# Kernel tuning notes

Hardware: AMD Instinct MI355X
Metric: run time of the kernel (lower is better)

## Reference

```python
import jax, jax.numpy as jnp
import numpy as np

BN_EPS = 1e-5


def sparsemax(z):
    # z: [B, D]; sparse projection onto the simplex along last axis.
    D = z.shape[-1]
    z_sorted = jnp.flip(jnp.sort(z, axis=-1), axis=-1)          # descending
    cs = jnp.cumsum(z_sorted, axis=-1)                           # cumulative sums
    k = jnp.arange(1, D + 1, dtype=z.dtype)                      # 1..D
    support = (1.0 + k * z_sorted) > cs                          # support condition
    k_star = jnp.sum(support, axis=-1, keepdims=True)            # support size, int
    cs_k = jnp.take_along_axis(cs, k_star - 1, axis=-1)
    tau = (cs_k - 1.0) / k_star.astype(z.dtype)                  # threshold
    return jnp.maximum(z - tau, 0.0)


def setup_inputs() -> dict:
    key = jax.random.key(0)
    k1, k2, k3 = jax.random.split(key, 3)
    B, D = 32768, 1024
    a = jax.random.normal(k1, (B, D), dtype=jnp.float32)
    p = jax.random.uniform(k2, (B, D), dtype=jnp.float32)        # prior scales in (0,1)
    W = jax.random.normal(k3, (D, D), dtype=jnp.float32) * (1.0 / np.sqrt(D))
    b = jnp.zeros((D,), dtype=jnp.float32)
    gamma = jnp.ones((D,), dtype=jnp.float32)
    beta = jnp.zeros((D,), dtype=jnp.float32)
    return {"a": a, "p": p, "W": W, "b": b, "gamma": gamma, "beta": beta}


def reference(a, p, W, b, gamma, beta):
    # Linear: a @ W^T + b  (torch nn.Linear convention)
    h = jnp.einsum("bd,ed->be", a, W) + b
    # BatchNorm1d (training mode: batch stats, biased variance)
    mean = jnp.mean(h, axis=0)
    var = jnp.mean(jnp.square(h - mean), axis=0)
    h = (h - mean) * jax.lax.rsqrt(var + BN_EPS) * gamma + beta
    # Prior scaling, then sparsemax -> attention mask
    mask = sparsemax(p * h)
    return mask
```

## Files before the change

### kernel.cpp

```cpp
#include <hip/hip_runtime.h>
#include <hip/hip_fp16.h>
#include <stdint.h>

typedef _Float16 f16x8 __attribute__((ext_vector_type(8)));
typedef float f32x4 __attribute__((ext_vector_type(4)));

#define BM 128
#define BN 128
#define BK 64

__device__ __forceinline__ void async_copy16(const void* g, void* l) {
  __builtin_amdgcn_global_load_lds(
      (__attribute__((address_space(1))) void*)(g),
      (__attribute__((address_space(3))) void*)(l),
      16, 0, 0);
}

__global__ __launch_bounds__(256) void cvt_f32_f16(const float* __restrict__ in,
                                                   _Float16* __restrict__ out,
                                                   size_t n) {
  size_t i = ((size_t)blockIdx.x * 256 + threadIdx.x) * 8;
  if (i + 8 > n) return;
  float4 u = *(const float4*)(in + i);
  float4 v = *(const float4*)(in + i + 4);
  f16x8 h;
  h[0] = (_Float16)u.x; h[1] = (_Float16)u.y; h[2] = (_Float16)u.z; h[3] = (_Float16)u.w;
  h[4] = (_Float16)v.x; h[5] = (_Float16)v.y; h[6] = (_Float16)v.z; h[7] = (_Float16)v.w;
  *(f16x8*)(out + i) = h;
}

template <bool DIRECT>
__global__ __launch_bounds__(256) void gemm_f16(const _Float16* __restrict__ Ah,
                                                const _Float16* __restrict__ Wh,
                                                const float* __restrict__ Af,
                                                const float* __restrict__ Wf,
                                                const float* __restrict__ bias,
                                                float* __restrict__ C,
                                                float* __restrict__ sum,
                                                float* __restrict__ sumsq,
                                                int M, int N, int K) {
  __shared__ __attribute__((aligned(16))) _Float16 lsA[BM * BK];
  __shared__ __attribute__((aligned(16))) _Float16 lsB[BN * BK];

  const int tid  = threadIdx.x;
  const int wave = tid >> 6;
  const int lane = tid & 63;
  const int wrow = (wave >> 1) * 64;
  const int wcol = (wave & 1) * 64;
  const int l16  = lane & 15;
  const int quad = lane >> 4;
  const int bm = blockIdx.y * BM;
  const int bn = blockIdx.x * BN;

  f32x4 acc[4][4];
#pragma unroll
  for (int i = 0; i < 4; ++i)
#pragma unroll
    for (int j = 0; j < 4; ++j) acc[i][j] = (f32x4){0.f, 0.f, 0.f, 0.f};

  for (int k0 = 0; k0 < K; k0 += BK) {
    if constexpr (DIRECT) {
#pragma unroll
      for (int i = 0; i < 4; ++i) {
        const int basechunk = i * 256 + wave * 64;
        const int g   = basechunk + lane;
        const int row = g >> 3;
        const int kc  = ((g & 7) ^ (row & 7)) << 3;
        async_copy16(Ah + (size_t)(bm + row) * K + k0 + kc, &lsA[basechunk * 8]);
        async_copy16(Wh + (size_t)(bn + row) * K + k0 + kc, &lsB[basechunk * 8]);
      }
    } else {
#pragma unroll
      for (int i = 0; i < 4; ++i) {
        const int g   = i * 256 + tid;
        const int row = g >> 3;
        const int kc  = ((g & 7) ^ (row & 7)) << 3;
        {
          const float* src = Af + (size_t)(bm + row) * K + k0 + kc;
          float4 u = *(const float4*)src;
          float4 v = *(const float4*)(src + 4);
          f16x8 h;
          h[0] = (_Float16)u.x; h[1] = (_Float16)u.y; h[2] = (_Float16)u.z; h[3] = (_Float16)u.w;
          h[4] = (_Float16)v.x; h[5] = (_Float16)v.y; h[6] = (_Float16)v.z; h[7] = (_Float16)v.w;
          *(f16x8*)&lsA[g * 8] = h;
        }
        {
          const float* src = Wf + (size_t)(bn + row) * K + k0 + kc;
          float4 u = *(const float4*)src;
          float4 v = *(const float4*)(src + 4);
          f16x8 h;
          h[0] = (_Float16)u.x; h[1] = (_Float16)u.y; h[2] = (_Float16)u.z; h[3] = (_Float16)u.w;
          h[4] = (_Float16)v.x; h[5] = (_Float16)v.y; h[6] = (_Float16)v.z; h[7] = (_Float16)v.w;
          *(f16x8*)&lsB[g * 8] = h;
        }
      }
    }
    __syncthreads();

#pragma unroll
    for (int kk = 0; kk < BK; kk += 32) {
      f16x8 af[4], bf[4];
#pragma unroll
      for (int i = 0; i < 4; ++i) {
        const int r = wrow + i * 16 + l16;
        const int col = ((kk >> 3) + quad) ^ (l16 & 7);
        af[i] = *(const f16x8*)&lsA[r * 64 + col * 8];
      }
#pragma unroll
      for (int j = 0; j < 4; ++j) {
        const int r = wcol + j * 16 + l16;
        const int col = ((kk >> 3) + quad) ^ (l16 & 7);
        bf[j] = *(const f16x8*)&lsB[r * 64 + col * 8];
      }
#pragma unroll
      for (int i = 0; i < 4; ++i)
#pragma unroll
        for (int j = 0; j < 4; ++j)
          acc[i][j] = __builtin_amdgcn_mfma_f32_16x16x32_f16(af[i], bf[j], acc[i][j], 0, 0, 0);
    }
    __syncthreads();
  }

#pragma unroll
  for (int j = 0; j < 4; ++j) {
    const int c = bn + wcol + j * 16 + l16;
    const float bv = bias[c];
    float s = 0.f, s2 = 0.f;
#pragma unroll
    for (int i = 0; i < 4; ++i) {
      const int r = bm + wrow + i * 16 + quad * 4;
      float* Cp = C + (size_t)r * N + c;
      f32x4 v = acc[i][j];
#pragma unroll
      for (int rr = 0; rr < 4; ++rr) {
        float val = v[rr] + bv;
        Cp[(size_t)rr * N] = val;
        s += val;
        s2 += val * val;
      }
    }
    s  += __shfl_xor(s, 16, 64);  s  += __shfl_xor(s, 32, 64);
    s2 += __shfl_xor(s2, 16, 64); s2 += __shfl_xor(s2, 32, 64);
    if (quad == 0) {
      atomicAdd(&sum[c], s);
      atomicAdd(&sumsq[c], s2);
    }
  }
}

__global__ __launch_bounds__(256) void bn_finalize(const float* __restrict__ sum,
                                                   const float* __restrict__ sumsq,
                                                   const float* __restrict__ gamma,
                                                   const float* __restrict__ beta,
                                                   float* __restrict__ scale,
                                                   float* __restrict__ shift,
                                                   float invB) {
  const int c = blockIdx.x * 256 + threadIdx.x;
  float mean = sum[c] * invB;
  float var  = sumsq[c] * invB - mean * mean;
  float rstd = rsqrtf(var + 1e-5f);
  float sc = rstd * gamma[c];
  scale[c] = sc;
  shift[c] = beta[c] - mean * sc;
}

__global__ __launch_bounds__(256) void bn_sparsemax(const float* H,
                                                    const float* __restrict__ P,
                                                    const float* __restrict__ scale,
                                                    const float* __restrict__ shift,
                                                    float* out, int D) {
  const int wave = threadIdx.x >> 6;
  const int lane = threadIdx.x & 63;
  const int row = blockIdx.x * 4 + wave;
  const size_t rowoff = (size_t)row * D;

  const f32x4* H4 = (const f32x4*)(H + rowoff);
  const f32x4* P4 = (const f32x4*)(P + rowoff);
  const f32x4* SC = (const f32x4*)scale;
  const f32x4* SH = (const f32x4*)shift;

  f32x4 z[4];
  float tot = 0.f;
#pragma unroll
  for (int j = 0; j < 4; ++j) {
    const int idx = j * 64 + lane;
    f32x4 zz = P4[idx] * (H4[idx] * SC[idx] + SH[idx]);
    z[j] = zz;
    tot += zz[0] + zz[1] + zz[2] + zz[3];
  }
#pragma unroll
  for (int o = 32; o > 0; o >>= 1) tot += __shfl_xor(tot, o, 64);

  float tau = (tot - 1.0f) / (float)D;
  float kprev = -1.0f;
  for (int it = 0; it < 64; ++it) {
    float s = 0.f, kf = 0.f;
#pragma unroll
    for (int j = 0; j < 4; ++j)
#pragma unroll
      for (int c = 0; c < 4; ++c) {
        float zz = z[j][c];
        if (zz > tau) { s += zz; kf += 1.0f; }
      }
#pragma unroll
    for (int o = 32; o > 0; o >>= 1) {
      s  += __shfl_xor(s, o, 64);
      kf += __shfl_xor(kf, o, 64);
    }
    tau = (s - 1.0f) / kf;
    if (kf == kprev) break;
    kprev = kf;
  }

  f32x4* O4 = (f32x4*)(out + rowoff);
#pragma unroll
  for (int j = 0; j < 4; ++j) {
    const int idx = j * 64 + lane;
    f32x4 o;
#pragma unroll
    for (int c = 0; c < 4; ++c) o[c] = fmaxf(z[j][c] - tau, 0.f);
    O4[idx] = o;
  }
}

extern "C" void kernel_launch(void* const* d_in, const int* in_sizes, int n_in,
                              void* d_out, int out_size, void* d_ws, size_t ws_size,
                              hipStream_t stream) {
  const float* a     = (const float*)d_in[0];
  const float* p     = (const float*)d_in[1];
  const float* W     = (const float*)d_in[2];
  const float* b     = (const float*)d_in[3];
  const float* gamma = (const float*)d_in[4];
  const float* beta  = (const float*)d_in[5];
  float* out = (float*)d_out;

  const int D = in_sizes[3];
  const int Brows = in_sizes[0] / D;
  const int K = D, N = D;

  float* wsum   = (float*)d_ws;
  float* wsumsq = wsum + D;
  float* wscale = wsum + 2 * D;
  float* wshift = wsum + 3 * D;
  _Float16* Ah = (_Float16*)((char*)d_ws + 16384);
  _Float16* Wh = Ah + (size_t)Brows * D;
  const size_t need = 16384 + ((size_t)Brows * D + (size_t)D * D) * sizeof(_Float16);
  const bool direct = ws_size >= need;

  hipMemsetAsync(d_ws, 0, 2 * D * sizeof(float), stream);

  if (direct) {
    const size_t na = (size_t)Brows * D;
    const size_t nw = (size_t)D * D;
    cvt_f32_f16<<<dim3((unsigned)(na / 8 / 256)), 256, 0, stream>>>(a, Ah, na);
    cvt_f32_f16<<<dim3((unsigned)(nw / 8 / 256)), 256, 0, stream>>>(W, Wh, nw);
    gemm_f16<true><<<dim3(N / BN, Brows / BM), 256, 0, stream>>>(
        Ah, Wh, nullptr, nullptr, b, out, wsum, wsumsq, Brows, N, K);
  } else {
    gemm_f16<false><<<dim3(N / BN, Brows / BM), 256, 0, stream>>>(
        nullptr, nullptr, a, W, b, out, wsum, wsumsq, Brows, N, K);
  }

  bn_finalize<<<dim3(D / 256), 256, 0, stream>>>(wsum, wsumsq, gamma, beta, wscale, wshift,
                                                 1.0f / (float)Brows);
  bn_sparsemax<<<dim3(Brows / 4), 256, 0, stream>>>(out, p, wscale, wshift, out, D);
}
```

Baseline: 464.1 us.

## Store GEMM output as fp16, replace stat atomics with partials, remap tiles per XCD

The GEMM now writes the pre-BN activations as fp16 into a workspace buffer, so the write and the later read in the sparsemax kernel move half as many bytes. Per-column sum and sum-of-squares atomics are replaced by per-tile partial slots, which a new finalize kernel reduces. This also removes the memset. Block indices are remapped so that consecutive M-tiles land on the same XCD, to improve L2 reuse. Rounding H to fp16 adds precision loss before the batch-norm and sparsemax steps.

```diff
diff --git a/kernel.cpp b/kernel.cpp
--- a/kernel.cpp
+++ b/kernel.cpp
@@ -3,6 +3,7 @@
 #include <stdint.h>
 
 typedef _Float16 f16x8 __attribute__((ext_vector_type(8)));
+typedef _Float16 f16x4 __attribute__((ext_vector_type(4)));
 typedef float f32x4 __attribute__((ext_vector_type(4)));
 
 #define BM 128
@@ -29,19 +30,117 @@
   *(f16x8*)(out + i) = h;
 }
 
-template <bool DIRECT>
-__global__ __launch_bounds__(256) void gemm_f16(const _Float16* __restrict__ Ah,
-                                                const _Float16* __restrict__ Wh,
-                                                const float* __restrict__ Af,
-                                                const float* __restrict__ Wf,
-                                                const float* __restrict__ bias,
-                                                float* __restrict__ C,
-                                                float* __restrict__ sum,
-                                                float* __restrict__ sumsq,
-                                                int M, int N, int K) {
+template <bool H16>
+__global__ __launch_bounds__(256) void gemm_direct(const _Float16* __restrict__ Ah,
+                                                   const _Float16* __restrict__ Wh,
+                                                   const float* __restrict__ bias,
+                                                   void* __restrict__ Hout,
+                                                   float* __restrict__ psum,
+                                                   float* __restrict__ psumsq,
+                                                   int M, int N, int K) {
   __shared__ __attribute__((aligned(16))) _Float16 lsA[BM * BK];
   __shared__ __attribute__((aligned(16))) _Float16 lsB[BN * BK];
 
+  const int tid  = threadIdx.x;
+  const int wave = tid >> 6;
+  const int lane = tid & 63;
+  const int wrow = (wave >> 1) * 64;
+  const int wcol = (wave & 1) * 64;
+  const int l16  = lane & 15;
+  const int quad = lane >> 4;
+
+  const int nx = gridDim.x;
+  const int li = blockIdx.y * nx + blockIdx.x;
+  const int xcd = li & 7;
+  const int jj  = li >> 3;
+  const int bnT = jj % nx;
+  const int bmT = xcd + (jj / nx) * 8;
+  const int bm = bmT * BM;
+  const int bn = bnT * BN;
+
+  f32x4 acc[4][4];
+#pragma unroll
+  for (int i = 0; i < 4; ++i)
+#pragma unroll
+    for (int j = 0; j < 4; ++j) acc[i][j] = (f32x4){0.f, 0.f, 0.f, 0.f};
+
+  for (int k0 = 0; k0 < K; k0 += BK) {
+#pragma unroll
+    for (int i = 0; i < 4; ++i) {
+      const int basechunk = i * 256 + wave * 64;
+      const int g   = basechunk + lane;
+      const int row = g >> 3;
+      const int kc  = ((g & 7) ^ (row & 7)) << 3;
+      async_copy16(Ah + (size_t)(bm + row) * K + k0 + kc, &lsA[basechunk * 8]);
+      async_copy16(Wh + (size_t)(bn + row) * K + k0 + kc, &lsB[basechunk * 8]);
+    }
+    __syncthreads();
+
+#pragma unroll
+    for (int kk = 0; kk < BK; kk += 32) {
+      f16x8 af[4], bf[4];
+#pragma unroll
+      for (int i = 0; i < 4; ++i) {
+        const int r = wrow + i * 16 + l16;
+        const int col = ((kk >> 3) + quad) ^ (l16 & 7);
+        af[i] = *(const f16x8*)&lsA[r * 64 + col * 8];
+      }
+#pragma unroll
+      for (int j = 0; j < 4; ++j) {
+        const int r = wcol + j * 16 + l16;
+        const int col = ((kk >> 3) + quad) ^ (l16 & 7);
+        bf[j] = *(const f16x8*)&lsB[r * 64 + col * 8];
+      }
+#pragma unroll
+      for (int i = 0; i < 4; ++i)
+#pragma unroll
+        for (int j = 0; j < 4; ++j)
+          acc[i][j] = __builtin_amdgcn_mfma_f32_16x16x32_f16(af[i], bf[j], acc[i][j], 0, 0, 0);
+    }
+    __syncthreads();
+  }
+
+  const int PS = (M >> 7) * 2;
+#pragma unroll
+  for (int j = 0; j < 4; ++j) {
+    const int c = bn + wcol + j * 16 + l16;
+    const float bv = bias[c];
+    float s = 0.f, s2 = 0.f;
+#pragma unroll
+    for (int i = 0; i < 4; ++i) {
+      const int r = bm + wrow + i * 16 + quad * 4;
+      f32x4 v = acc[i][j];
+#pragma unroll
+      for (int rr = 0; rr < 4; ++rr) {
+        float val = v[rr] + bv;
+        if constexpr (H16) {
+          ((_Float16*)Hout)[(size_t)(r + rr) * N + c] = (_Float16)val;
+        } else {
+          ((float*)Hout)[(size_t)(r + rr) * N + c] = val;
+        }
+        s += val;
+        s2 += val * val;
+      }
+    }
+    s  += __shfl_xor(s, 16, 64);  s  += __shfl_xor(s, 32, 64);
+    s2 += __shfl_xor(s2, 16, 64); s2 += __shfl_xor(s2, 32, 64);
+    if (quad == 0) {
+      const size_t slot = (size_t)c * PS + bmT * 2 + (wave >> 1);
+      psum[slot] = s;
+      psumsq[slot] = s2;
+    }
+  }
+}
+
+__global__ __launch_bounds__(256) void gemm_fallback(const float* __restrict__ Af,
+                                                     const float* __restrict__ Wf,
+                                                     const float* __restrict__ bias,
+                                                     float* __restrict__ C,
+                                                     float* __restrict__ sum,
+                                                     float* __restrict__ sumsq,
+                                                     int M, int N, int K) {
+  __shared__ __attribute__((aligned(16))) _Float16 lsA[BM * BK];
+  __shared__ __attribute__((aligned(16))) _Float16 lsB[BN * BK];
   const int tid  = threadIdx.x;
   const int wave = tid >> 6;
   const int lane = tid & 63;
@@ -59,44 +158,31 @@
     for (int j = 0; j < 4; ++j) acc[i][j] = (f32x4){0.f, 0.f, 0.f, 0.f};
 
   for (int k0 = 0; k0 < K; k0 += BK) {
-    if constexpr (DIRECT) {
-#pragma unroll
-      for (int i = 0; i < 4; ++i) {
-        const int basechunk = i * 256 + wave * 64;
-        const int g   = basechunk + lane;
-        const int row = g >> 3;
-        const int kc  = ((g & 7) ^ (row & 7)) << 3;
-        async_copy16(Ah + (size_t)(bm + row) * K + k0 + kc, &lsA[basechunk * 8]);
-        async_copy16(Wh + (size_t)(bn + row) * K + k0 + kc, &lsB[basechunk * 8]);
-      }
-    } else {
-#pragma unroll
-      for (int i = 0; i < 4; ++i) {
-        const int g   = i * 256 + tid;
-        const int row = g >> 3;
-        const int kc  = ((g & 7) ^ (row & 7)) << 3;
-        {
-          const float* src = Af + (size_t)(bm + row) * K + k0 + kc;
-          float4 u = *(const float4*)src;
-          float4 v = *(const float4*)(src + 4);
-          f16x8 h;
-          h[0] = (_Float16)u.x; h[1] = (_Float16)u.y; h[2] = (_Float16)u.z; h[3] = (_Float16)u.w;
-          h[4] = (_Float16)v.x; h[5] = (_Float16)v.y; h[6] = (_Float16)v.z; h[7] = (_Float16)v.w;
-          *(f16x8*)&lsA[g * 8] = h;
-        }
-        {
-          const float* src = Wf + (size_t)(bn + row) * K + k0 + kc;
-          float4 u = *(const float4*)src;
-          float4 v = *(const float4*)(src + 4);
-          f16x8 h;
-          h[0] = (_Float16)u.x; h[1] = (_Float16)u.y; h[2] = (_Float16)u.z; h[3] = (_Float16)u.w;
-          h[4] = (_Float16)v.x; h[5] = (_Float16)v.y; h[6] = (_Float16)v.z; h[7] = (_Float16)v.w;
-          *(f16x8*)&lsB[g * 8] = h;
-        }
+#pragma unroll
+    for (int i = 0; i < 4; ++i) {
+      const int g   = i * 256 + tid;
+      const int row = g >> 3;
+      const int kc  = ((g & 7) ^ (row & 7)) << 3;
+      {
+        const float* src = Af + (size_t)(bm + row) * K + k0 + kc;
+        float4 u = *(const float4*)src;
+        float4 v = *(const float4*)(src + 4);
+        f16x8 h;
+        h[0] = (_Float16)u.x; h[1] = (_Float16)u.y; h[2] = (_Float16)u.z; h[3] = (_Float16)u.w;
+        h[4] = (_Float16)v.x; h[5] = (_Float16)v.y; h[6] = (_Float16)v.z; h[7] = (_Float16)v.w;
+        *(f16x8*)&lsA[g * 8] = h;
+      }
+      {
+        const float* src = Wf + (size_t)(bn + row) * K + k0 + kc;
+        float4 u = *(const float4*)src;
+        float4 v = *(const float4*)(src + 4);
+        f16x8 h;
+        h[0] = (_Float16)u.x; h[1] = (_Float16)u.y; h[2] = (_Float16)u.z; h[3] = (_Float16)u.w;
+        h[4] = (_Float16)v.x; h[5] = (_Float16)v.y; h[6] = (_Float16)v.z; h[7] = (_Float16)v.w;
+        *(f16x8*)&lsB[g * 8] = h;
       }
     }
     __syncthreads();
-
 #pragma unroll
     for (int kk = 0; kk < BK; kk += 32) {
       f16x8 af[4], bf[4];
@@ -145,6 +231,38 @@
       atomicAdd(&sum[c], s);
       atomicAdd(&sumsq[c], s2);
     }
+  }
+}
+
+__global__ __launch_bounds__(256) void bn_finalize_direct(const float* __restrict__ psum,
+                                                          const float* __restrict__ psumsq,
+                                                          const float* __restrict__ gamma,
+                                                          const float* __restrict__ beta,
+                                                          float* __restrict__ scale,
+                                                          float* __restrict__ shift,
+                                                          float invB, int PS) {
+  const int wave = threadIdx.x >> 6;
+  const int lane = threadIdx.x & 63;
+  const int c = blockIdx.x * 4 + wave;
+  const f32x4* ps = (const f32x4*)(psum + (size_t)c * PS);
+  const f32x4* pq = (const f32x4*)(psumsq + (size_t)c * PS);
+  float s = 0.f, q = 0.f;
+  for (int k = lane; k < (PS >> 2); k += 64) {
+    f32x4 v = ps[k]; s += v[0] + v[1] + v[2] + v[3];
+    f32x4 w = pq[k]; q += w[0] + w[1] + w[2] + w[3];
+  }
+#pragma unroll
+  for (int o = 32; o > 0; o >>= 1) {
+    s += __shfl_xor(s, o, 64);
+    q += __shfl_xor(q, o, 64);
+  }
+  if (lane == 0) {
+    float mean = s * invB;
+    float var  = q * invB - mean * mean;
+    float rstd = rsqrtf(var + 1e-5f);
+    float sc = rstd * gamma[c];
+    scale[c] = sc;
+    shift[c] = beta[c] - mean * sc;
   }
 }
 
@@ -164,7 +282,8 @@
   shift[c] = beta[c] - mean * sc;
 }
 
-__global__ __launch_bounds__(256) void bn_sparsemax(const float* H,
+template <bool H16>
+__global__ __launch_bounds__(256) void bn_sparsemax(const void* H,
                                                     const float* __restrict__ P,
                                                     const float* __restrict__ scale,
                                                     const float* __restrict__ shift,
@@ -174,7 +293,6 @@
   const int row = blockIdx.x * 4 + wave;
   const size_t rowoff = (size_t)row * D;
 
-  const f32x4* H4 = (const f32x4*)(H + rowoff);
   const f32x4* P4 = (const f32x4*)(P + rowoff);
   const f32x4* SC = (const f32x4*)scale;
   const f32x4* SH = (const f32x4*)shift;
@@ -184,7 +302,14 @@
 #pragma unroll
   for (int j = 0; j < 4; ++j) {
     const int idx = j * 64 + lane;
-    f32x4 zz = P4[idx] * (H4[idx] * SC[idx] + SH[idx]);
+    f32x4 hv;
+    if constexpr (H16) {
+      f16x4 h4 = ((const f16x4*)((const _Float16*)H + rowoff))[idx];
+      hv[0] = (float)h4[0]; hv[1] = (float)h4[1]; hv[2] = (float)h4[2]; hv[3] = (float)h4[3];
+    } else {
+      hv = ((const f32x4*)((const float*)H + rowoff))[idx];
+    }
+    f32x4 zz = P4[idx] * (hv * SC[idx] + SH[idx]);
     z[j] = zz;
     tot += zz[0] + zz[1] + zz[2] + zz[3];
   }
@@ -237,31 +362,51 @@
   const int D = in_sizes[3];
   const int Brows = in_sizes[0] / D;
   const int K = D, N = D;
-
-  float* wsum   = (float*)d_ws;
-  float* wsumsq = wsum + D;
-  float* wscale = wsum + 2 * D;
-  float* wshift = wsum + 3 * D;
-  _Float16* Ah = (_Float16*)((char*)d_ws + 16384);
-  _Float16* Wh = Ah + (size_t)Brows * D;
-  const size_t need = 16384 + ((size_t)Brows * D + (size_t)D * D) * sizeof(_Float16);
-  const bool direct = ws_size >= need;
-
-  hipMemsetAsync(d_ws, 0, 2 * D * sizeof(float), stream);
-
-  if (direct) {
-    const size_t na = (size_t)Brows * D;
-    const size_t nw = (size_t)D * D;
+  const size_t na = (size_t)Brows * D;
+  const size_t nw = (size_t)D * D;
+  const int PS = (Brows / BM) * 2;
+
+  const size_t statsB = (size_t)D * PS * sizeof(float);
+  float* psum   = (float*)d_ws;
+  float* psumsq = (float*)((char*)d_ws + statsB);
+  float* wscale = (float*)((char*)d_ws + 2 * statsB);
+  float* wshift = wscale + D;
+  const size_t off_Ah = 2 * statsB + 16384;
+  _Float16* Ah = (_Float16*)((char*)d_ws + off_Ah);
+  _Float16* Wh = Ah + na;
+  _Float16* Hh = Wh + nw;
+  const size_t need1 = off_Ah + (na + nw) * sizeof(_Float16);
+  const size_t need2 = need1 + na * sizeof(_Float16);
+
+  if (ws_size >= need1) {
     cvt_f32_f16<<<dim3((unsigned)(na / 8 / 256)), 256, 0, stream>>>(a, Ah, na);
     cvt_f32_f16<<<dim3((unsigned)(nw / 8 / 256)), 256, 0, stream>>>(W, Wh, nw);
-    gemm_f16<true><<<dim3(N / BN, Brows / BM), 256, 0, stream>>>(
-        Ah, Wh, nullptr, nullptr, b, out, wsum, wsumsq, Brows, N, K);
+    const bool h16 = ws_size >= need2;
+    if (h16) {
+      gemm_direct<true><<<dim3(N / BN, Brows / BM), 256, 0, stream>>>(
+          Ah, Wh, b, Hh, psum, psumsq, Brows, N, K);
+    } else {
+      gemm_direct<false><<<dim3(N / BN, Brows / BM), 256, 0, stream>>>(
+          Ah, Wh, b, out, psum, psumsq, Brows, N, K);
+    }
+    bn_finalize_direct<<<dim3(D / 4), 256, 0, stream>>>(psum, psumsq, gamma, beta,
+                                                        wscale, wshift,
+                                                        1.0f / (float)Brows, PS);
+    if (h16) {
+      bn_sparsemax<true><<<dim3(Brows / 4), 256, 0, stream>>>(Hh, p, wscale, wshift, out, D);
+    } else {
+      bn_sparsemax<false><<<dim3(Brows / 4), 256, 0, stream>>>(out, p, wscale, wshift, out, D);
+    }
   } else {
-    gemm_f16<false><<<dim3(N / BN, Brows / BM), 256, 0, stream>>>(
-        nullptr, nullptr, a, W, b, out, wsum, wsumsq, Brows, N, K);
-  }
-
-  bn_finalize<<<dim3(D / 256), 256, 0, stream>>>(wsum, wsumsq, gamma, beta, wscale, wshift,
-                                                 1.0f / (float)Brows);
-  bn_sparsemax<<<dim3(Brows / 4), 256, 0, stream>>>(out, p, wscale, wshift, out, D);
-}
+    float* wsum   = (float*)d_ws;
+    float* wsumsq = wsum + D;
+    float* fscale = wsum + 2 * D;
+    float* fshift = wsum + 3 * D;
+    hipMemsetAsync(d_ws, 0, 2 * D * sizeof(float), stream);
+    gemm_fallback<<<dim3(N / BN, Brows / BM), 256, 0, stream>>>(
+        a, W, b, out, wsum, wsumsq, Brows, N, K);
+    bn_finalize<<<dim3(D / 256), 256, 0, stream>>>(wsum, wsumsq, gamma, beta, fscale, fshift,
+                                                   1.0f / (float)Brows);
+    bn_sparsemax<false><<<dim3(Brows / 4), 256, 0, stream>>>(out, p, fscale, fshift, out, D);
+  }
+}
```

After: 437.5 us. 1.06x faster.
